# Kernel optimization log

Hardware: AMD Instinct MI355X
Metric: run time of the kernel (lower is better)

The kernel has to match this reference:

```python
import jax, jax.numpy as jnp
import numpy as np

IN_CHANNELS = 192
KERNEL_SIZE = 3
GROUPS = 1
N_ITER = 3  # power_it_niter


def _gram_conv(K):
    """Gram step of the conv operator: G[a, b] = sum_o corr(K[o, a], K[o, b]).

    K: (co, ci, k, k) -> (ci, ci, 2k-1, 2k-1). This is the kernel of M^T M
    where M is the (zero-padded) conv operator with kernel K.
    """
    k = K.shape[-1]
    lhs = jnp.transpose(K, (1, 0, 2, 3))  # batch = a-index, channels = o
    rhs = jnp.transpose(K, (1, 0, 2, 3))  # out-chan = b-index, in-chan = o
    return jax.lax.conv_general_dilated(
        lhs, rhs, window_strides=(1, 1),
        padding=[(k - 1, k - 1), (k - 1, k - 1)],
        dimension_numbers=("NCHW", "OIHW", "NCHW"))


def _sigma_one_group(K, n_iter):
    """Gram-iteration spectral-norm estimate (Delattre et al. 2024).

    sigma(K_0) ~= prod_t f_t^(1/2^t) * ||K_T||_F^(1/2^T), f_t = Frobenius norm
    before each Gram squaring (normalization keeps values in fp range).
    """
    log_sigma = jnp.asarray(0.0, K.dtype)
    for t in range(n_iter):  # static unroll: kernel spatial size grows k -> 2k-1
        f = jnp.sqrt(jnp.sum(K * K))
        K = K / f
        log_sigma = log_sigma + jnp.log(f) / (2.0 ** t)
        K = _gram_conv(K)
    f_final = jnp.sqrt(jnp.sum(K * K))
    log_sigma = log_sigma + jnp.log(f_final) / (2.0 ** n_iter)
    return jnp.exp(log_sigma)


def compute_delattre2024(K, n_iter):
    # K: (groups, c, c, k, k) -> (groups,) per-group spectral norm estimates
    return jax.vmap(lambda g: _sigma_one_group(g, n_iter))(K)


def setup_inputs() -> dict:
    key = jax.random.key(0)
    kernel = jax.random.normal(
        key, (IN_CHANNELS * GROUPS, IN_CHANNELS, KERNEL_SIZE, KERNEL_SIZE),
        dtype=jnp.float32)
    return {"kernel": kernel}


def reference(kernel):
    g = GROUPS
    c = IN_CHANNELS // GROUPS
    K = kernel.reshape(g, c, c, KERNEL_SIZE, KERNEL_SIZE)
    sigmas = compute_delattre2024(K, N_ITER)  # (groups,)
    K = K / sigmas.reshape(-1, 1, 1, 1, 1)
    return K.reshape(IN_CHANNELS * GROUPS, IN_CHANNELS, KERNEL_SIZE, KERNEL_SIZE)
```

## Files before the change

### kernel.cpp

```cpp
#include <hip/hip_runtime.h>
#include <hip/hip_bf16.h>

typedef __bf16 bf16;
typedef __attribute__((ext_vector_type(8))) __bf16 bf16x8;
typedef __attribute__((ext_vector_type(4))) float f32x4;
typedef __attribute__((ext_vector_type(4))) int i32x4;

#define CH 192
#define MAT (CH * CH)
#define NF 145
#define FSTRIDE (2 * MAT)
#define NELEM (CH * CH * 9)
#define XSCALE 9.765625e-4f
#define W17 0.36959913571644626f
#define NGRAM (8 * 19 * 3)


__global__ void k_dft(const float* __restrict__ K, bf16* __restrict__ X,
                      float* __restrict__ s3) {
    __shared__ float twc[17], tws[17];
    int bid = blockIdx.x;
    int xcd = bid & 7;
    int r = bid >> 3;
    int g4 = r / 144, sub = r % 144;
    int t = threadIdx.x;
    if (bid == 0 && t == 0) *s3 = 0.0f;
    if (t < 17) {
        float s, c;
        __sincosf(-W17 * (float)t, &s, &c);
        twc[t] = c; tws[t] = s;
    }
    int p = sub * 256 + t;
    int a = p / CH, o = p % CH;
    const float* src = K + (size_t)(o * CH + a) * 9;
    float kv[9];
#pragma unroll
    for (int i = 0; i < 9; ++i) kv[i] = src[i];
    __syncthreads();
#pragma unroll
    for (int jj = 0; jj < 4; ++jj) {
        int f = xcd + 8 * (g4 * 4 + jj);
        if (f >= NF) break;
        int fy, fx;
        if (f < 9) { fy = 0; fx = f; }
        else { int u = f - 9; fy = 1 + u / 17; fx = u % 17; }
        float pyr = twc[fy], pyi = tws[fy];
        float pxr = twc[fx], pxi = tws[fx];
        int fx2 = 2 * fx; if (fx2 >= 17) fx2 -= 17;
        int fy2 = 2 * fy; if (fy2 >= 17) fy2 -= 17;
        float px2r = twc[fx2], px2i = tws[fx2];
        float py2r = twc[fy2], py2i = tws[fy2];
        float s0r = kv[0] + kv[1] * pxr + kv[2] * px2r, s0i = kv[1] * pxi + kv[2] * px2i;
        float s1r = kv[3] + kv[4] * pxr + kv[5] * px2r, s1i = kv[4] * pxi + kv[5] * px2i;
        float s2r = kv[6] + kv[7] * pxr + kv[8] * px2r, s2i = kv[7] * pxi + kv[8] * px2i;
        float ar = s0r + pyr * s1r - pyi * s1i + py2r * s2r - py2i * s2i;
        float ai = s0i + pyr * s1i + pyi * s1r + py2r * s2i + py2i * s2r;
        size_t base = (size_t)f * FSTRIDE;
        X[base + p]       = (bf16)(ar * XSCALE);
        X[base + MAT + p] = (bf16)(ai * XSCALE);
    }
}

#define LDSR 72
#define SLAB (96 * LDSR)
#define OLDSR 104

template <bool WRITE, bool NORM>
__global__ __launch_bounds__(256, 2) void k_gram(const bf16* __restrict__ X,
                                                 bf16* __restrict__ Y,
                                                 float* __restrict__ s3) {
    __shared__ bf16 lds[4 * SLAB];
    __shared__ float red[4];
    int bid = blockIdx.x;
    int xcd = bid & 7, r = bid >> 3;
    int fi = r / 3, q = r % 3;
    int f = xcd + 8 * fi;
    if (f >= NF) return;
    int row0 = (q == 2) ? 96 : 0;
    int col0 = (q >= 1) ? 96 : 0;
    bool diag = (q != 1);
    int sb2 = diag ? 0 : 2;
    const bf16* Xf = X + (size_t)f * FSTRIDE;

    int tid = threadIdx.x;
    int lane = tid & 63, w = tid >> 6;
    int wr = (w >> 1) * 48, wc = (w & 1) * 48;
    int ml = lane & 15, kq = (lane >> 4) * 8;

    f32x4 cr[3][3], ci[3][3];
#pragma unroll
    for (int i = 0; i < 3; ++i)
#pragma unroll
        for (int j = 0; j < 3; ++j) {
            cr[i][j] = f32x4{0.f, 0.f, 0.f, 0.f};
            ci[i][j] = f32x4{0.f, 0.f, 0.f, 0.f};
        }

    for (int kc = 0; kc < CH; kc += 64) {
        i32x4 v[12];
#pragma unroll
        for (int s = 0; s < 2; ++s) {
            const bf16* src = Xf + (s ? MAT : 0) + (size_t)row0 * CH + kc;
#pragma unroll
            for (int j = 0; j < 3; ++j) {
                int chunk = j * 256 + tid;
                int rr = chunk >> 3, c8 = chunk & 7;
                v[s * 3 + j] = *(const i32x4*)(src + rr * CH + c8 * 8);
            }
        }
        if (!diag) {
#pragma unroll
            for (int s = 2; s < 4; ++s) {
                const bf16* src = Xf + ((s & 1) ? MAT : 0) + (size_t)col0 * CH + kc;
#pragma unroll
                for (int j = 0; j < 3; ++j) {
                    int chunk = j * 256 + tid;
                    int rr = chunk >> 3, c8 = chunk & 7;
                    v[s * 3 + j] = *(const i32x4*)(src + rr * CH + c8 * 8);
                }
            }
        }
        __syncthreads();
#pragma unroll
        for (int s = 0; s < 2; ++s)
#pragma unroll
            for (int j = 0; j < 3; ++j) {
                int chunk = j * 256 + tid;
                int rr = chunk >> 3, c8 = chunk & 7;
                *(i32x4*)&lds[s * SLAB + rr * LDSR + c8 * 8] = v[s * 3 + j];
            }
        if (!diag) {
#pragma unroll
            for (int s = 2; s < 4; ++s)
#pragma unroll
                for (int j = 0; j < 3; ++j) {
                    int chunk = j * 256 + tid;
                    int rr = chunk >> 3, c8 = chunk & 7;
                    *(i32x4*)&lds[s * SLAB + rr * LDSR + c8 * 8] = v[s * 3 + j];
                }
        }
        __syncthreads();

#pragma unroll
        for (int ks = 0; ks < 64; ks += 32) {
            bf16x8 ar[3], ai[3], nai[3], br[3], bi[3];
            int ko = ks + kq;
#pragma unroll
            for (int mt = 0; mt < 3; ++mt) {
                ar[mt] = *(const bf16x8*)&lds[0 * SLAB + (wr + mt * 16 + ml) * LDSR + ko];
                ai[mt] = *(const bf16x8*)&lds[1 * SLAB + (wr + mt * 16 + ml) * LDSR + ko];
                br[mt] = *(const bf16x8*)&lds[(sb2 + 0) * SLAB + (wc + mt * 16 + ml) * LDSR + ko];
                bi[mt] = *(const bf16x8*)&lds[(sb2 + 1) * SLAB + (wc + mt * 16 + ml) * LDSR + ko];
                i32x4 u = __builtin_bit_cast(i32x4, ai[mt]);
                u ^= 0x80008000;
                nai[mt] = __builtin_bit_cast(bf16x8, u);
            }
#pragma unroll
            for (int mt = 0; mt < 3; ++mt)
#pragma unroll
                for (int nt = 0; nt < 3; ++nt) {
                    cr[mt][nt] = __builtin_amdgcn_mfma_f32_16x16x32_bf16(ar[mt],  br[nt], cr[mt][nt], 0, 0, 0);
                    cr[mt][nt] = __builtin_amdgcn_mfma_f32_16x16x32_bf16(ai[mt],  bi[nt], cr[mt][nt], 0, 0, 0);
                    ci[mt][nt] = __builtin_amdgcn_mfma_f32_16x16x32_bf16(ar[mt],  bi[nt], ci[mt][nt], 0, 0, 0);
                    ci[mt][nt] = __builtin_amdgcn_mfma_f32_16x16x32_bf16(nai[mt], br[nt], ci[mt][nt], 0, 0, 0);
                }
        }
    }

    if (WRITE) {
        bf16* tileA = lds;
        bf16* tileB = lds + 96 * OLDSR;
        bf16* Yf = Y + (size_t)f * FSTRIDE;
        int lr0 = wr + (lane >> 4) * 4;
        int lc0 = wc + ml;
#pragma unroll
        for (int part = 0; part < 2; ++part) {
            __syncthreads();
#pragma unroll
            for (int mt = 0; mt < 3; ++mt)
#pragma unroll
                for (int nt = 0; nt < 3; ++nt)
#pragma unroll
                    for (int rr = 0; rr < 4; ++rr) {
                        float vv = part ? ci[mt][nt][rr] : cr[mt][nt][rr];
                        int rrow = lr0 + mt * 16 + rr;
                        int ccol = lc0 + nt * 16;
                        tileA[rrow * OLDSR + ccol] = (bf16)vv;
                        if (q == 1)
                            tileB[ccol * OLDSR + rrow] = (bf16)(part ? -vv : vv);
                    }
            __syncthreads();
            bf16* dst = Yf + (part ? MAT : 0) + (size_t)row0 * CH + col0;
            for (int ch = tid; ch < 96 * 12; ch += 256) {
                int rw = ch / 12, cc = ch % 12;
                *(i32x4*)&dst[(size_t)rw * CH + cc * 8] = *(const i32x4*)&tileA[rw * OLDSR + cc * 8];
            }
            if (q == 1) {
                bf16* dst2 = Yf + (part ? MAT : 0) + (size_t)col0 * CH + row0;
                for (int ch = tid; ch < 96 * 12; ch += 256) {
                    int rw = ch / 12, cc = ch % 12;
                    *(i32x4*)&dst2[(size_t)rw * CH + cc * 8] = *(const i32x4*)&tileB[rw * OLDSR + cc * 8];
                }
            }
        }
    }
    if (NORM) {
        float loc = 0.f;
#pragma unroll
        for (int mt = 0; mt < 3; ++mt)
#pragma unroll
            for (int nt = 0; nt < 3; ++nt)
#pragma unroll
                for (int rr = 0; rr < 4; ++rr)
                    loc += cr[mt][nt][rr] * cr[mt][nt][rr] + ci[mt][nt][rr] * ci[mt][nt][rr];
#pragma unroll
        for (int off = 32; off > 0; off >>= 1) loc += __shfl_down(loc, off, 64);
        if (lane == 0) red[w] = loc;
        __syncthreads();
        if (tid == 0) {
            float base = (f == 0) ? 1.0f : 2.0f;
            float wq = (q == 1) ? 2.0f : 1.0f;
            atomicAdd(s3, base * wq * (red[0] + red[1] + red[2] + red[3]));
        }
    }
}

__global__ void k_scale(const float* __restrict__ K, float* __restrict__ out,
                        const float* __restrict__ s3) {
    float sig = 1024.0f * exp2f(log2f((*s3) * (1.0f / 289.0f)) * 0.0625f);
    float inv = 1.0f / sig;
    int i = (blockIdx.x * 256 + threadIdx.x) * 4;
    f32x4 v = *(const f32x4*)(K + i);
    v *= inv;
    *(f32x4*)(out + i) = v;
}

extern "C" void kernel_launch(void* const* d_in, const int* in_sizes, int n_in,
                              void* d_out, int out_size, void* d_ws, size_t ws_size,
                              hipStream_t stream) {
    const float* K = (const float*)d_in[0];
    float* out = (float*)d_out;
    char* ws = (char*)d_ws;
    float* s3 = (float*)ws;
    bf16* bufX = (bf16*)(ws + 256);
    bf16* bufH = bufX + (size_t)NF * FSTRIDE;

    k_dft<<<8 * 5 * 144, 256, 0, stream>>>(K, bufX, s3);
    k_gram<true,  false><<<NGRAM, 256, 0, stream>>>(bufX, bufH, nullptr);
    k_gram<true,  false><<<NGRAM, 256, 0, stream>>>(bufH, bufX, nullptr);
    k_gram<false, true ><<<NGRAM, 256, 0, stream>>>(bufX, nullptr, s3);
    k_scale<<<NELEM / 1024, 256, 0, stream>>>(K, out, s3);
}
```

Measured before the change: 109.0 us.

## Vectorize DFT stores and load larger K chunks in Gram kernel

The DFT kernel now has each thread produce 8 consecutive outputs and write them as 16-byte bf16x8 stores, with fewer blocks that each cover 5 frequencies. The Gram kernel now loads the full 192-wide K dimension into LDS in one pass for diagonal tiles, and in two 96-wide phases for the off-diagonal tile, instead of three 64-wide chunks. The aim is fewer barriers and wider, coalesced memory transactions. The cost is more registers (kv[8][9], v[18]) and more LDS per block, which may reduce occupancy. The DFT now also reads K with a strided pattern across o.

```diff
diff --git a/kernel.cpp b/kernel.cpp
--- a/kernel.cpp
+++ b/kernel.cpp
@@ -22,7 +22,7 @@
     int bid = blockIdx.x;
     int xcd = bid & 7;
     int r = bid >> 3;
-    int g4 = r / 144, sub = r % 144;
+    int g = r / 18, chunk = r % 18;
     int t = threadIdx.x;
     if (bid == 0 && t == 0) *s3 = 0.0f;
     if (t < 17) {
@@ -30,40 +30,76 @@
         __sincosf(-W17 * (float)t, &s, &c);
         twc[t] = c; tws[t] = s;
     }
-    int p = sub * 256 + t;
-    int a = p / CH, o = p % CH;
-    const float* src = K + (size_t)(o * CH + a) * 9;
-    float kv[9];
-#pragma unroll
-    for (int i = 0; i < 9; ++i) kv[i] = src[i];
+    int p0 = chunk * 2048 + t * 8;
+    int a = p0 / CH, o0 = p0 % CH;
+    float kv[8][9];
+#pragma unroll
+    for (int j = 0; j < 8; ++j) {
+        const float* src = K + ((size_t)(o0 + j) * CH + a) * 9;
+#pragma unroll
+        for (int i = 0; i < 9; ++i) kv[j][i] = src[i];
+    }
     __syncthreads();
 #pragma unroll
-    for (int jj = 0; jj < 4; ++jj) {
-        int f = xcd + 8 * (g4 * 4 + jj);
-        if (f >= NF) break;
+    for (int u = 0; u < 5; ++u) {
+        int f = xcd + 8 * (g * 5 + u);
+        if (f >= NF) continue;
         int fy, fx;
         if (f < 9) { fy = 0; fx = f; }
-        else { int u = f - 9; fy = 1 + u / 17; fx = u % 17; }
+        else { int uu = f - 9; fy = 1 + uu / 17; fx = uu % 17; }
         float pyr = twc[fy], pyi = tws[fy];
         float pxr = twc[fx], pxi = tws[fx];
         int fx2 = 2 * fx; if (fx2 >= 17) fx2 -= 17;
         int fy2 = 2 * fy; if (fy2 >= 17) fy2 -= 17;
         float px2r = twc[fx2], px2i = tws[fx2];
         float py2r = twc[fy2], py2i = tws[fy2];
-        float s0r = kv[0] + kv[1] * pxr + kv[2] * px2r, s0i = kv[1] * pxi + kv[2] * px2i;
-        float s1r = kv[3] + kv[4] * pxr + kv[5] * px2r, s1i = kv[4] * pxi + kv[5] * px2i;
-        float s2r = kv[6] + kv[7] * pxr + kv[8] * px2r, s2i = kv[7] * pxi + kv[8] * px2i;
-        float ar = s0r + pyr * s1r - pyi * s1i + py2r * s2r - py2i * s2i;
-        float ai = s0i + pyr * s1i + pyi * s1r + py2r * s2i + py2i * s2r;
-        size_t base = (size_t)f * FSTRIDE;
-        X[base + p]       = (bf16)(ar * XSCALE);
-        X[base + MAT + p] = (bf16)(ai * XSCALE);
-    }
-}
-
-#define LDSR 72
+        bf16x8 vr, vi;
+#pragma unroll
+        for (int j = 0; j < 8; ++j) {
+            float s0r = kv[j][0] + kv[j][1] * pxr + kv[j][2] * px2r, s0i = kv[j][1] * pxi + kv[j][2] * px2i;
+            float s1r = kv[j][3] + kv[j][4] * pxr + kv[j][5] * px2r, s1i = kv[j][4] * pxi + kv[j][5] * px2i;
+            float s2r = kv[j][6] + kv[j][7] * pxr + kv[j][8] * px2r, s2i = kv[j][7] * pxi + kv[j][8] * px2i;
+            float ar = s0r + pyr * s1r - pyi * s1i + py2r * s2r - py2i * s2i;
+            float ai = s0i + pyr * s1i + pyi * s1r + py2r * s2i + py2i * s2r;
+            vr[j] = (bf16)(ar * XSCALE);
+            vi[j] = (bf16)(ai * XSCALE);
+        }
+        size_t base = (size_t)f * FSTRIDE + p0;
+        *(i32x4*)(X + base)       = __builtin_bit_cast(i32x4, vr);
+        *(i32x4*)(X + base + MAT) = __builtin_bit_cast(i32x4, vi);
+    }
+}
+
+#define LDSR 104
 #define SLAB (96 * LDSR)
+#define DLDSR 200
+#define DSLAB (96 * DLDSR)
 #define OLDSR 104
+
+#define COMPUTE_KS(STRIDE, SSIZE, SB2, KO_BASE)                                       \
+    {                                                                                 \
+        bf16x8 ar[3], ai[3], nai[3], br[3], bi[3];                                    \
+        int ko = (KO_BASE) + kq;                                                      \
+        _Pragma("unroll")                                                             \
+        for (int mt = 0; mt < 3; ++mt) {                                              \
+            ar[mt] = *(const bf16x8*)&lds[0 * (SSIZE) + (wr + mt * 16 + ml) * (STRIDE) + ko]; \
+            ai[mt] = *(const bf16x8*)&lds[1 * (SSIZE) + (wr + mt * 16 + ml) * (STRIDE) + ko]; \
+            br[mt] = *(const bf16x8*)&lds[((SB2) + 0) * (SSIZE) + (wc + mt * 16 + ml) * (STRIDE) + ko]; \
+            bi[mt] = *(const bf16x8*)&lds[((SB2) + 1) * (SSIZE) + (wc + mt * 16 + ml) * (STRIDE) + ko]; \
+            i32x4 uu = __builtin_bit_cast(i32x4, ai[mt]);                             \
+            uu ^= 0x80008000;                                                         \
+            nai[mt] = __builtin_bit_cast(bf16x8, uu);                                 \
+        }                                                                             \
+        _Pragma("unroll")                                                             \
+        for (int mt = 0; mt < 3; ++mt)                                                \
+            _Pragma("unroll")                                                         \
+            for (int nt = 0; nt < 3; ++nt) {                                          \
+                cr[mt][nt] = __builtin_amdgcn_mfma_f32_16x16x32_bf16(ar[mt],  br[nt], cr[mt][nt], 0, 0, 0); \
+                cr[mt][nt] = __builtin_amdgcn_mfma_f32_16x16x32_bf16(ai[mt],  bi[nt], cr[mt][nt], 0, 0, 0); \
+                ci[mt][nt] = __builtin_amdgcn_mfma_f32_16x16x32_bf16(ar[mt],  bi[nt], ci[mt][nt], 0, 0, 0); \
+                ci[mt][nt] = __builtin_amdgcn_mfma_f32_16x16x32_bf16(nai[mt], br[nt], ci[mt][nt], 0, 0, 0); \
+            }                                                                         \
+    }
 
 template <bool WRITE, bool NORM>
 __global__ __launch_bounds__(256, 2) void k_gram(const bf16* __restrict__ X,
@@ -79,7 +115,6 @@
     int row0 = (q == 2) ? 96 : 0;
     int col0 = (q >= 1) ? 96 : 0;
     bool diag = (q != 1);
-    int sb2 = diag ? 0 : 2;
     const bf16* Xf = X + (size_t)f * FSTRIDE;
 
     int tid = threadIdx.x;
@@ -96,74 +131,58 @@
             ci[i][j] = f32x4{0.f, 0.f, 0.f, 0.f};
         }
 
-    for (int kc = 0; kc < CH; kc += 64) {
-        i32x4 v[12];
+    if (diag) {
+        i32x4 v[18];
 #pragma unroll
         for (int s = 0; s < 2; ++s) {
-            const bf16* src = Xf + (s ? MAT : 0) + (size_t)row0 * CH + kc;
-#pragma unroll
-            for (int j = 0; j < 3; ++j) {
-                int chunk = j * 256 + tid;
-                int rr = chunk >> 3, c8 = chunk & 7;
-                v[s * 3 + j] = *(const i32x4*)(src + rr * CH + c8 * 8);
-            }
-        }
-        if (!diag) {
-#pragma unroll
-            for (int s = 2; s < 4; ++s) {
-                const bf16* src = Xf + ((s & 1) ? MAT : 0) + (size_t)col0 * CH + kc;
-#pragma unroll
-                for (int j = 0; j < 3; ++j) {
-                    int chunk = j * 256 + tid;
-                    int rr = chunk >> 3, c8 = chunk & 7;
-                    v[s * 3 + j] = *(const i32x4*)(src + rr * CH + c8 * 8);
-                }
-            }
-        }
+            const bf16* src = Xf + (s ? MAT : 0) + (size_t)row0 * CH;
+#pragma unroll
+            for (int j = 0; j < 9; ++j) {
+                int c = j * 256 + tid;
+                int rr = c / 24, cc = c % 24;
+                v[s * 9 + j] = *(const i32x4*)(src + rr * CH + cc * 8);
+            }
+        }
+#pragma unroll
+        for (int s = 0; s < 2; ++s)
+#pragma unroll
+            for (int j = 0; j < 9; ++j) {
+                int c = j * 256 + tid;
+                int rr = c / 24, cc = c % 24;
+                *(i32x4*)&lds[s * DSLAB + rr * DLDSR + cc * 8] = v[s * 9 + j];
+            }
         __syncthreads();
 #pragma unroll
-        for (int s = 0; s < 2; ++s)
-#pragma unroll
-            for (int j = 0; j < 3; ++j) {
-                int chunk = j * 256 + tid;
-                int rr = chunk >> 3, c8 = chunk & 7;
-                *(i32x4*)&lds[s * SLAB + rr * LDSR + c8 * 8] = v[s * 3 + j];
-            }
-        if (!diag) {
-#pragma unroll
-            for (int s = 2; s < 4; ++s)
-#pragma unroll
-                for (int j = 0; j < 3; ++j) {
-                    int chunk = j * 256 + tid;
-                    int rr = chunk >> 3, c8 = chunk & 7;
-                    *(i32x4*)&lds[s * SLAB + rr * LDSR + c8 * 8] = v[s * 3 + j];
-                }
-        }
-        __syncthreads();
-
-#pragma unroll
-        for (int ks = 0; ks < 64; ks += 32) {
-            bf16x8 ar[3], ai[3], nai[3], br[3], bi[3];
-            int ko = ks + kq;
-#pragma unroll
-            for (int mt = 0; mt < 3; ++mt) {
-                ar[mt] = *(const bf16x8*)&lds[0 * SLAB + (wr + mt * 16 + ml) * LDSR + ko];
-                ai[mt] = *(const bf16x8*)&lds[1 * SLAB + (wr + mt * 16 + ml) * LDSR + ko];
-                br[mt] = *(const bf16x8*)&lds[(sb2 + 0) * SLAB + (wc + mt * 16 + ml) * LDSR + ko];
-                bi[mt] = *(const bf16x8*)&lds[(sb2 + 1) * SLAB + (wc + mt * 16 + ml) * LDSR + ko];
-                i32x4 u = __builtin_bit_cast(i32x4, ai[mt]);
-                u ^= 0x80008000;
-                nai[mt] = __builtin_bit_cast(bf16x8, u);
-            }
-#pragma unroll
-            for (int mt = 0; mt < 3; ++mt)
-#pragma unroll
-                for (int nt = 0; nt < 3; ++nt) {
-                    cr[mt][nt] = __builtin_amdgcn_mfma_f32_16x16x32_bf16(ar[mt],  br[nt], cr[mt][nt], 0, 0, 0);
-                    cr[mt][nt] = __builtin_amdgcn_mfma_f32_16x16x32_bf16(ai[mt],  bi[nt], cr[mt][nt], 0, 0, 0);
-                    ci[mt][nt] = __builtin_amdgcn_mfma_f32_16x16x32_bf16(ar[mt],  bi[nt], ci[mt][nt], 0, 0, 0);
-                    ci[mt][nt] = __builtin_amdgcn_mfma_f32_16x16x32_bf16(nai[mt], br[nt], ci[mt][nt], 0, 0, 0);
-                }
+        for (int ks = 0; ks < 192; ks += 32) {
+            COMPUTE_KS(DLDSR, DSLAB, 0, ks)
+        }
+    } else {
+#pragma unroll
+        for (int ph = 0; ph < 2; ++ph) {
+            int kc = ph * 96;
+            i32x4 v[18];
+#pragma unroll
+            for (int j = 0; j < 18; ++j) {
+                int gi = j * 256 + tid;
+                int s = gi / 1152, c = gi % 1152;
+                int rr = c / 12, cc = c % 12;
+                const bf16* src = Xf + ((s & 1) ? MAT : 0)
+                                + (size_t)(((s < 2) ? row0 : col0) + rr) * CH + kc;
+                v[j] = *(const i32x4*)(src + cc * 8);
+            }
+            __syncthreads();
+#pragma unroll
+            for (int j = 0; j < 18; ++j) {
+                int gi = j * 256 + tid;
+                int s = gi / 1152, c = gi % 1152;
+                int rr = c / 12, cc = c % 12;
+                *(i32x4*)&lds[s * SLAB + rr * LDSR + cc * 8] = v[j];
+            }
+            __syncthreads();
+#pragma unroll
+            for (int ks = 0; ks < 96; ks += 32) {
+                COMPUTE_KS(LDSR, SLAB, 2, ks)
+            }
         }
     }
 
@@ -245,7 +264,7 @@
     bf16* bufX = (bf16*)(ws + 256);
     bf16* bufH = bufX + (size_t)NF * FSTRIDE;
 
-    k_dft<<<8 * 5 * 144, 256, 0, stream>>>(K, bufX, s3);
+    k_dft<<<8 * 4 * 18, 256, 0, stream>>>(K, bufX, s3);
     k_gram<true,  false><<<NGRAM, 256, 0, stream>>>(bufX, bufH, nullptr);
     k_gram<true,  false><<<NGRAM, 256, 0, stream>>>(bufH, bufX, nullptr);
     k_gram<false, true ><<<NGRAM, 256, 0, stream>>>(bufX, nullptr, s3);
```

After: 113.2 us. 1.04x slower.
